# Kernel optimization log

Hardware: AMD Instinct MI355X
Metric: run time of the kernel (lower is better)

## Reference

```python
import jax, jax.numpy as jnp
import numpy as np

B, R, S, H = 4, 64, 512, 768
E = 64            # candidate entities per example
SEG = 128         # seg_emb_dim
NT, NC, NP = 6, 13, 3
REP = 3 * H + 2 * SEG  # rel_rep_size = 2560
NEG = -1e30


def setup_inputs() -> dict:
    key = jax.random.key(0)
    ks = jax.random.split(key, 12)
    hidden_states = jax.random.normal(ks[0], (B, S, H), dtype=jnp.float32)
    rel_pairs = jax.random.randint(ks[1], (B, R, 2), 0, E, dtype=jnp.int64)
    rel_masks = jax.random.randint(ks[2], (B, R, S), 0, 2, dtype=jnp.int32)
    rel_sizes = jax.random.randint(ks[3], (B, R, 2), 0, 30, dtype=jnp.int64)
    ent_span_reps = jax.random.normal(ks[4], (B, E, H), dtype=jnp.float32)
    ent_segs_embs = jax.random.normal(ks[5], (B, E, SEG), dtype=jnp.float32)
    s = 1.0 / np.sqrt(REP)
    W_type = jax.random.uniform(ks[6], (REP, NT), jnp.float32, -s, s)
    b_type = jax.random.uniform(ks[7], (NT,), jnp.float32, -s, s)
    W_cate = jax.random.uniform(ks[8], (REP, NC), jnp.float32, -s, s)
    b_cate = jax.random.uniform(ks[9], (NC,), jnp.float32, -s, s)
    W_pola = jax.random.uniform(ks[10], (REP, NP), jnp.float32, -s, s)
    b_pola = jax.random.uniform(ks[11], (NP,), jnp.float32, -s, s)
    return {"hidden_states": hidden_states, "rel_pairs": rel_pairs,
            "rel_masks": rel_masks, "rel_sizes": rel_sizes,
            "ent_span_reps": ent_span_reps, "ent_segs_embs": ent_segs_embs,
            "W_type": W_type, "b_type": b_type, "W_cate": W_cate,
            "b_cate": b_cate, "W_pola": W_pola, "b_pola": b_pola}


def reference(hidden_states, rel_pairs, rel_masks, rel_sizes,
              ent_span_reps, ent_segs_embs,
              W_type, b_type, W_cate, b_cate, W_pola, b_pola):
    batch, max_rels, _ = rel_pairs.shape
    # batched gather: ent_span_reps[b, rel_pairs[b]] -> [B, R, 2, H] -> [B, R, 2H]
    pair_span = jnp.take_along_axis(
        ent_span_reps[:, :, None, :],
        rel_pairs[:, None, :, :, None].reshape(batch, max_rels * 2, 1, 1), axis=1
    ).reshape(batch, max_rels, -1)
    pair_segs = jnp.take_along_axis(
        ent_segs_embs[:, :, None, :],
        rel_pairs[:, None, :, :, None].reshape(batch, max_rels * 2, 1, 1), axis=1
    ).reshape(batch, max_rels, -1)
    # masked max over seq: scores [B, R, S, H]
    mask_add = (rel_masks == 0).astype(jnp.float32) * NEG          # [B, R, S]
    ctx = jnp.max(hidden_states[:, None, :, :] + mask_add[..., None], axis=2)  # [B, R, H]
    has_ctx = jnp.any(rel_masks != 0, axis=-1)                      # [B, R]
    ctx = jnp.where(has_ctx[..., None], ctx, 0.0)
    features = jnp.concatenate([pair_span, pair_segs, ctx], axis=2)  # [B, R, 2560]
    # dropout is identity at inference
    rel_type_logits = features @ W_type + b_type
    rel_cate_logits = features @ W_cate + b_cate
    rel_pola_logits = features @ W_pola + b_pola
    return (rel_type_logits, rel_cate_logits, rel_pola_logits)
```

## Files before the change

kernel.cpp:

```cpp
#include <hip/hip_runtime.h>
#include <math.h>

#define BB 4
#define RR 64
#define SS 512
#define HH 768
#define EE 64
#define SEGD 128
#define NT 6
#define NC 13
#define NP 3
#define NO (NT + NC + NP)
#define REP 2560
#define RPG 8
#define NGRP (RR / RPG)
#define NEGV -1e30f

template<int ROWS>
__global__ __launch_bounds__(192)
void p1_maxctx(const float* __restrict__ hidden,
               const int*   __restrict__ rel_masks,
               float* __restrict__ ws)
{
    constexpr int SC = SS / ROWS;
    const int bid  = blockIdx.x;
    const int sc   = bid % SC;
    const int grp  = (bid / SC) % NGRP;
    const int b    = bid / (SC * NGRP);
    const int t    = threadIdx.x;
    const int s0   = sc * ROWS;
    const int r0   = grp * RPG;

    __shared__ float sadd[RPG * ROWS];

    for (int i = t; i < RPG * ROWS; i += 192) {
        const int r = i / ROWS;
        const int s = i - r * ROWS;
        const int mv = rel_masks[((size_t)(b * RR + r0 + r)) * SS + s0 + s];
        sadd[i] = mv ? 0.f : NEGV;
    }
    __syncthreads();

    float4 m[RPG];
#pragma unroll
    for (int r = 0; r < RPG; ++r)
        m[r] = make_float4(-INFINITY, -INFINITY, -INFINITY, -INFINITY);

#pragma unroll 8
    for (int s = 0; s < ROWS; ++s) {
        const float4 v = *reinterpret_cast<const float4*>(
            hidden + ((size_t)(b * SS + s0 + s)) * HH + 4 * t);
#pragma unroll
        for (int r = 0; r < RPG; ++r) {
            const float a = sadd[r * ROWS + s];
            m[r].x = fmaxf(m[r].x, v.x + a);
            m[r].y = fmaxf(m[r].y, v.y + a);
            m[r].z = fmaxf(m[r].z, v.z + a);
            m[r].w = fmaxf(m[r].w, v.w + a);
        }
    }

#pragma unroll
    for (int r = 0; r < RPG; ++r) {
        float* wp = ws + (((size_t)(b * RR + r0 + r) * SC) + sc) * HH;
        *reinterpret_cast<float4*>(wp + 4 * t) = m[r];
    }
}

__global__ __launch_bounds__(256)
void p2_head(const float* __restrict__ ws,
             const int*   __restrict__ rel_pairs,
             const float* __restrict__ span,
             const float* __restrict__ segs,
             const float* __restrict__ Wt, const float* __restrict__ bt,
             const float* __restrict__ Wc, const float* __restrict__ bc,
             const float* __restrict__ Wp, const float* __restrict__ bp,
             float* __restrict__ out, int SC)
{
    const int br = blockIdx.x;
    const int b  = br / RR;
    const int t  = threadIdx.x;

    __shared__ float feat[REP];
    __shared__ float red[4][NO];

    const int i0 = rel_pairs[(size_t)br * 2 + 0];
    const int i1 = rel_pairs[(size_t)br * 2 + 1];

    if (t < 192) {
        const float* sp0 = span + ((size_t)b * EE + i0) * HH;
        const float* sp1 = span + ((size_t)b * EE + i1) * HH;
        *reinterpret_cast<float4*>(&feat[4 * t]) =
            *reinterpret_cast<const float4*>(sp0 + 4 * t);
        *reinterpret_cast<float4*>(&feat[HH + 4 * t]) =
            *reinterpret_cast<const float4*>(sp1 + 4 * t);
    } else {
        const int u = t - 192;
        const float* sg = (u < 32) ? (segs + ((size_t)b * EE + i0) * SEGD)
                                   : (segs + ((size_t)b * EE + i1) * SEGD);
        const int v = (u < 32) ? u : (u - 32);
        *reinterpret_cast<float4*>(&feat[2 * HH + ((u < 32) ? 0 : SEGD) + 4 * v]) =
            *reinterpret_cast<const float4*>(sg + 4 * v);
    }

    if (t < 192) {
        float4 mm = make_float4(-INFINITY, -INFINITY, -INFINITY, -INFINITY);
#pragma unroll 4
        for (int c = 0; c < SC; ++c) {
            const float4 w = *reinterpret_cast<const float4*>(
                ws + ((size_t)br * SC + c) * HH + 4 * t);
            mm.x = fmaxf(mm.x, w.x);
            mm.y = fmaxf(mm.y, w.y);
            mm.z = fmaxf(mm.z, w.z);
            mm.w = fmaxf(mm.w, w.w);
        }
        if (mm.x < -1e29f) mm.x = 0.f;
        if (mm.y < -1e29f) mm.y = 0.f;
        if (mm.z < -1e29f) mm.z = 0.f;
        if (mm.w < -1e29f) mm.w = 0.f;
        const int CTX0 = 2 * HH + 2 * SEGD;
        *reinterpret_cast<float4*>(&feat[CTX0 + 4 * t]) = mm;
    }
    __syncthreads();

    float acc[NO];
#pragma unroll
    for (int o = 0; o < NO; ++o) acc[o] = 0.f;
    for (int f = t; f < REP; f += 256) {
        const float fv = feat[f];
        const float* wt = Wt + (size_t)f * NT;
        const float* wc = Wc + (size_t)f * NC;
        const float* wp = Wp + (size_t)f * NP;
#pragma unroll
        for (int o = 0; o < NT; ++o) acc[o]           += fv * wt[o];
#pragma unroll
        for (int o = 0; o < NC; ++o) acc[NT + o]      += fv * wc[o];
#pragma unroll
        for (int o = 0; o < NP; ++o) acc[NT + NC + o] += fv * wp[o];
    }
#pragma unroll
    for (int o = 0; o < NO; ++o) {
#pragma unroll
        for (int off = 32; off > 0; off >>= 1)
            acc[o] += __shfl_down(acc[o], off, 64);
    }
    const int wid  = t >> 6;
    const int lane = t & 63;
    if (lane == 0) {
#pragma unroll
        for (int o = 0; o < NO; ++o) red[wid][o] = acc[o];
    }
    __syncthreads();

    if (t < NO) {
        const float v = red[0][t] + red[1][t] + red[2][t] + red[3][t];
        if (t < NT) {
            out[(size_t)br * NT + t] = v + bt[t];
        } else if (t < NT + NC) {
            const int o = t - NT;
            out[(size_t)BB * RR * NT + (size_t)br * NC + o] = v + bc[o];
        } else {
            const int o = t - NT - NC;
            out[(size_t)BB * RR * (NT + NC) + (size_t)br * NP + o] = v + bp[o];
        }
    }
}

__global__ __launch_bounds__(256)
void rel_cls_fused(const float* __restrict__ hidden,
                   const int*   __restrict__ rel_pairs,
                   const int*   __restrict__ rel_masks,
                   const float* __restrict__ span,
                   const float* __restrict__ segs,
                   const float* __restrict__ Wt, const float* __restrict__ bt,
                   const float* __restrict__ Wc, const float* __restrict__ bc,
                   const float* __restrict__ Wp, const float* __restrict__ bp,
                   float* __restrict__ out)
{
    const int br = blockIdx.x;
    const int b  = br / RR;
    const int t  = threadIdx.x;

    __shared__ float sadd[SS];
    __shared__ float feat[REP];
    __shared__ float red[4][NO];

    const int* mrow = rel_masks + (size_t)br * SS;
    sadd[t]       = mrow[t] ? 0.f : NEGV;
    sadd[t + 256] = mrow[t + 256] ? 0.f : NEGV;

    const int i0 = rel_pairs[(size_t)br * 2 + 0];
    const int i1 = rel_pairs[(size_t)br * 2 + 1];
    const float* sp0 = span + ((size_t)b * EE + i0) * HH;
    const float* sp1 = span + ((size_t)b * EE + i1) * HH;
    feat[t]            = sp0[t];
    feat[t + 256]      = sp0[t + 256];
    feat[t + 512]      = sp0[t + 512];
    feat[HH + t]       = sp1[t];
    feat[HH + t + 256] = sp1[t + 256];
    feat[HH + t + 512] = sp1[t + 512];
    const float* sg0 = segs + ((size_t)b * EE + i0) * SEGD;
    const float* sg1 = segs + ((size_t)b * EE + i1) * SEGD;
    if (t < SEGD) feat[2 * HH + t] = sg0[t];
    else          feat[2 * HH + SEGD + (t - SEGD)] = sg1[t - SEGD];
    __syncthreads();

    float m0 = -INFINITY, m1 = -INFINITY, m2 = -INFINITY;
#pragma unroll 4
    for (int s = 0; s < SS; ++s) {
        const float* hp = hidden + ((size_t)b * SS + s) * HH;
        const float a = sadd[s];
        m0 = fmaxf(m0, hp[t] + a);
        m1 = fmaxf(m1, hp[t + 256] + a);
        m2 = fmaxf(m2, hp[t + 512] + a);
    }
    if (m0 < -1e29f) m0 = 0.f;
    if (m1 < -1e29f) m1 = 0.f;
    if (m2 < -1e29f) m2 = 0.f;
    const int CTX0 = 2 * HH + 2 * SEGD;
    feat[CTX0 + t]       = m0;
    feat[CTX0 + t + 256] = m1;
    feat[CTX0 + t + 512] = m2;
    __syncthreads();

    float acc[NO];
#pragma unroll
    for (int o = 0; o < NO; ++o) acc[o] = 0.f;
    for (int f = t; f < REP; f += 256) {
        const float fv = feat[f];
        const float* wt = Wt + (size_t)f * NT;
        const float* wc = Wc + (size_t)f * NC;
        const float* wp = Wp + (size_t)f * NP;
#pragma unroll
        for (int o = 0; o < NT; ++o) acc[o]           += fv * wt[o];
#pragma unroll
        for (int o = 0; o < NC; ++o) acc[NT + o]      += fv * wc[o];
#pragma unroll
        for (int o = 0; o < NP; ++o) acc[NT + NC + o] += fv * wp[o];
    }
#pragma unroll
    for (int o = 0; o < NO; ++o) {
#pragma unroll
        for (int off = 32; off > 0; off >>= 1)
            acc[o] += __shfl_down(acc[o], off, 64);
    }
    const int wid  = t >> 6;
    const int lane = t & 63;
    if (lane == 0) {
#pragma unroll
        for (int o = 0; o < NO; ++o) red[wid][o] = acc[o];
    }
    __syncthreads();

    if (t < NO) {
        const float v = red[0][t] + red[1][t] + red[2][t] + red[3][t];
        if (t < NT) {
            out[(size_t)br * NT + t] = v + bt[t];
        } else if (t < NT + NC) {
            const int o = t - NT;
            out[(size_t)BB * RR * NT + (size_t)br * NC + o] = v + bc[o];
        } else {
            const int o = t - NT - NC;
            out[(size_t)BB * RR * (NT + NC) + (size_t)br * NP + o] = v + bp[o];
        }
    }
}

extern "C" void kernel_launch(void* const* d_in, const int* in_sizes, int n_in,
                              void* d_out, int out_size, void* d_ws, size_t ws_size,
                              hipStream_t stream) {
    const float* hidden = (const float*)d_in[0];
    const int*   pairs  = (const int*)d_in[1];
    const int*   masks  = (const int*)d_in[2];
    const float* span   = (const float*)d_in[4];
    const float* segs   = (const float*)d_in[5];
    const float* Wt     = (const float*)d_in[6];
    const float* bt     = (const float*)d_in[7];
    const float* Wc     = (const float*)d_in[8];
    const float* bc     = (const float*)d_in[9];
    const float* Wp     = (const float*)d_in[10];
    const float* bp     = (const float*)d_in[11];
    float* out = (float*)d_out;

    const size_t slot = (size_t)BB * RR * HH * sizeof(float);
    float* ws = (float*)d_ws;

    int SC = 0;
    if      ((size_t)32 * slot <= ws_size) SC = 32;
    else if ((size_t)16 * slot <= ws_size) SC = 16;
    else if ((size_t) 8 * slot <= ws_size) SC = 8;
    else if ((size_t) 4 * slot <= ws_size) SC = 4;

    if (SC) {
        dim3 g1(BB * NGRP * SC), b1(192);
        switch (SC) {
            case 32: hipLaunchKernelGGL((p1_maxctx<SS/32>), g1, b1, 0, stream, hidden, masks, ws); break;
            case 16: hipLaunchKernelGGL((p1_maxctx<SS/16>), g1, b1, 0, stream, hidden, masks, ws); break;
            case  8: hipLaunchKernelGGL((p1_maxctx<SS/ 8>), g1, b1, 0, stream, hidden, masks, ws); break;
            default: hipLaunchKernelGGL((p1_maxctx<SS/ 4>), g1, b1, 0, stream, hidden, masks, ws); break;
        }
        dim3 g2(BB * RR), b2(256);
        hipLaunchKernelGGL(p2_head, g2, b2, 0, stream, ws, pairs, span, segs,
                           Wt, bt, Wc, bc, Wp, bp, out, SC);
    } else {
        dim3 grid(BB * RR), blk(256);
        hipLaunchKernelGGL(rel_cls_fused, grid, blk, 0, stream,
                           hidden, pairs, masks, span, segs,
                           Wt, bt, Wc, bc, Wp, bp, out);
    }
}
```

Measured before the change: 33.51 us.

## Transpose classifier weights in phase one and fix split count at sixteen

Extra blocks in the first kernel transpose the three classifier weight matrices into an output-major workspace, so the head kernel can read contiguous float4 weight rows per output instead of strided scalar loads. The masked-max kernel now uses 256 threads with three scalar columns each, and the sequence split is fixed at 16 chunks. Span and segment gathers in the head are moved onto the otherwise idle fourth wave so they overlap the partial-max reduction. The weights are re-transposed on every call, which adds work and workspace traffic to the first kernel, and the two-kernel path now requires a larger workspace.

```diff
diff --git a/kernel.cpp b/kernel.cpp
--- a/kernel.cpp
+++ b/kernel.cpp
@@ -15,55 +15,79 @@
 #define RPG 8
 #define NGRP (RR / RPG)
 #define NEGV -1e30f
-
-template<int ROWS>
-__global__ __launch_bounds__(192)
+#define SCQ 16
+#define ROWS (SS / SCQ)
+#define NB1 (BB * NGRP * SCQ)
+#define NTB 64
+#define WT_ELEMS (REP * NO)
+#define OFF_WT ((size_t)BB * RR * SCQ * HH)
+
+__global__ __launch_bounds__(256)
 void p1_maxctx(const float* __restrict__ hidden,
                const int*   __restrict__ rel_masks,
+               const float* __restrict__ Wt,
+               const float* __restrict__ Wc,
+               const float* __restrict__ Wp,
                float* __restrict__ ws)
 {
-    constexpr int SC = SS / ROWS;
-    const int bid  = blockIdx.x;
-    const int sc   = bid % SC;
-    const int grp  = (bid / SC) % NGRP;
-    const int b    = bid / (SC * NGRP);
-    const int t    = threadIdx.x;
-    const int s0   = sc * ROWS;
-    const int r0   = grp * RPG;
+    const int bid = blockIdx.x;
+    const int t   = threadIdx.x;
+
+    if (bid >= NB1) {
+        float* WT = ws + OFF_WT;
+        for (int e = (bid - NB1) * 256 + t; e < WT_ELEMS; e += NTB * 256) {
+            const int o = e / REP;
+            const int f = e - o * REP;
+            float v;
+            if (o < NT)           v = Wt[(size_t)f * NT + o];
+            else if (o < NT + NC) v = Wc[(size_t)f * NC + (o - NT)];
+            else                  v = Wp[(size_t)f * NP + (o - NT - NC)];
+            WT[e] = v;
+        }
+        return;
+    }
+
+    const int sc  = bid % SCQ;
+    const int grp = (bid / SCQ) % NGRP;
+    const int b   = bid / (SCQ * NGRP);
+    const int s0  = sc * ROWS;
+    const int r0  = grp * RPG;
 
     __shared__ float sadd[RPG * ROWS];
-
-    for (int i = t; i < RPG * ROWS; i += 192) {
-        const int r = i / ROWS;
-        const int s = i - r * ROWS;
+    {
+        const int r = t / ROWS;
+        const int s = t - r * ROWS;
         const int mv = rel_masks[((size_t)(b * RR + r0 + r)) * SS + s0 + s];
-        sadd[i] = mv ? 0.f : NEGV;
-    }
-    __syncthreads();
-
-    float4 m[RPG];
-#pragma unroll
-    for (int r = 0; r < RPG; ++r)
-        m[r] = make_float4(-INFINITY, -INFINITY, -INFINITY, -INFINITY);
-
+        sadd[t] = mv ? 0.f : NEGV;
+    }
+    __syncthreads();
+
+    float m[RPG][3];
+#pragma unroll
+    for (int r = 0; r < RPG; ++r) { m[r][0] = -INFINITY; m[r][1] = -INFINITY; m[r][2] = -INFINITY; }
+
+    const float* hbase = hidden + ((size_t)b * SS + s0) * HH + t;
 #pragma unroll 8
     for (int s = 0; s < ROWS; ++s) {
-        const float4 v = *reinterpret_cast<const float4*>(
-            hidden + ((size_t)(b * SS + s0 + s)) * HH + 4 * t);
+        const float* hp = hbase + (size_t)s * HH;
+        const float v0 = hp[0];
+        const float v1 = hp[256];
+        const float v2 = hp[512];
 #pragma unroll
         for (int r = 0; r < RPG; ++r) {
             const float a = sadd[r * ROWS + s];
-            m[r].x = fmaxf(m[r].x, v.x + a);
-            m[r].y = fmaxf(m[r].y, v.y + a);
-            m[r].z = fmaxf(m[r].z, v.z + a);
-            m[r].w = fmaxf(m[r].w, v.w + a);
+            m[r][0] = fmaxf(m[r][0], v0 + a);
+            m[r][1] = fmaxf(m[r][1], v1 + a);
+            m[r][2] = fmaxf(m[r][2], v2 + a);
         }
     }
 
 #pragma unroll
     for (int r = 0; r < RPG; ++r) {
-        float* wp = ws + (((size_t)(b * RR + r0 + r) * SC) + sc) * HH;
-        *reinterpret_cast<float4*>(wp + 4 * t) = m[r];
+        float* wp = ws + (((size_t)(b * RR + r0 + r)) * SCQ + sc) * HH + t;
+        wp[0]   = m[r][0];
+        wp[256] = m[r][1];
+        wp[512] = m[r][2];
     }
 }
 
@@ -72,10 +96,10 @@
              const int*   __restrict__ rel_pairs,
              const float* __restrict__ span,
              const float* __restrict__ segs,
-             const float* __restrict__ Wt, const float* __restrict__ bt,
-             const float* __restrict__ Wc, const float* __restrict__ bc,
-             const float* __restrict__ Wp, const float* __restrict__ bp,
-             float* __restrict__ out, int SC)
+             const float* __restrict__ bt,
+             const float* __restrict__ bc,
+             const float* __restrict__ bp,
+             float* __restrict__ out)
 {
     const int br = blockIdx.x;
     const int b  = br / RR;
@@ -86,29 +110,14 @@
 
     const int i0 = rel_pairs[(size_t)br * 2 + 0];
     const int i1 = rel_pairs[(size_t)br * 2 + 1];
-
-    if (t < 192) {
-        const float* sp0 = span + ((size_t)b * EE + i0) * HH;
-        const float* sp1 = span + ((size_t)b * EE + i1) * HH;
-        *reinterpret_cast<float4*>(&feat[4 * t]) =
-            *reinterpret_cast<const float4*>(sp0 + 4 * t);
-        *reinterpret_cast<float4*>(&feat[HH + 4 * t]) =
-            *reinterpret_cast<const float4*>(sp1 + 4 * t);
-    } else {
-        const int u = t - 192;
-        const float* sg = (u < 32) ? (segs + ((size_t)b * EE + i0) * SEGD)
-                                   : (segs + ((size_t)b * EE + i1) * SEGD);
-        const int v = (u < 32) ? u : (u - 32);
-        *reinterpret_cast<float4*>(&feat[2 * HH + ((u < 32) ? 0 : SEGD) + 4 * v]) =
-            *reinterpret_cast<const float4*>(sg + 4 * v);
-    }
+    const int CTX0 = 2 * HH + 2 * SEGD;
 
     if (t < 192) {
         float4 mm = make_float4(-INFINITY, -INFINITY, -INFINITY, -INFINITY);
-#pragma unroll 4
-        for (int c = 0; c < SC; ++c) {
-            const float4 w = *reinterpret_cast<const float4*>(
-                ws + ((size_t)br * SC + c) * HH + 4 * t);
+        const float* wbase = ws + (size_t)br * SCQ * HH + 4 * t;
+#pragma unroll
+        for (int c = 0; c < SCQ; ++c) {
+            const float4 w = *reinterpret_cast<const float4*>(wbase + (size_t)c * HH);
             mm.x = fmaxf(mm.x, w.x);
             mm.y = fmaxf(mm.y, w.y);
             mm.z = fmaxf(mm.z, w.z);
@@ -118,26 +127,53 @@
         if (mm.y < -1e29f) mm.y = 0.f;
         if (mm.z < -1e29f) mm.z = 0.f;
         if (mm.w < -1e29f) mm.w = 0.f;
-        const int CTX0 = 2 * HH + 2 * SEGD;
         *reinterpret_cast<float4*>(&feat[CTX0 + 4 * t]) = mm;
-    }
-    __syncthreads();
+    } else {
+        for (int k = t - 192; k < 448; k += 64) {
+            float4 v; int dst;
+            if (k < 192) {
+                v = *reinterpret_cast<const float4*>(span + ((size_t)b * EE + i0) * HH + 4 * k);
+                dst = 4 * k;
+            } else if (k < 384) {
+                const int u = k - 192;
+                v = *reinterpret_cast<const float4*>(span + ((size_t)b * EE + i1) * HH + 4 * u);
+                dst = HH + 4 * u;
+            } else if (k < 416) {
+                const int u = k - 384;
+                v = *reinterpret_cast<const float4*>(segs + ((size_t)b * EE + i0) * SEGD + 4 * u);
+                dst = 2 * HH + 4 * u;
+            } else {
+                const int u = k - 416;
+                v = *reinterpret_cast<const float4*>(segs + ((size_t)b * EE + i1) * SEGD + 4 * u);
+                dst = 2 * HH + SEGD + 4 * u;
+            }
+            *reinterpret_cast<float4*>(&feat[dst]) = v;
+        }
+    }
+    __syncthreads();
+
+    const float* WT = ws + OFF_WT;
+    const float4 f0 = *reinterpret_cast<const float4*>(&feat[4 * t]);
+    const float4 f1 = *reinterpret_cast<const float4*>(&feat[4 * t + 1024]);
+    const bool has2 = (t < 128);
+    float4 f2 = make_float4(0.f, 0.f, 0.f, 0.f);
+    if (has2) f2 = *reinterpret_cast<const float4*>(&feat[4 * t + 2048]);
 
     float acc[NO];
-#pragma unroll
-    for (int o = 0; o < NO; ++o) acc[o] = 0.f;
-    for (int f = t; f < REP; f += 256) {
-        const float fv = feat[f];
-        const float* wt = Wt + (size_t)f * NT;
-        const float* wc = Wc + (size_t)f * NC;
-        const float* wp = Wp + (size_t)f * NP;
-#pragma unroll
-        for (int o = 0; o < NT; ++o) acc[o]           += fv * wt[o];
-#pragma unroll
-        for (int o = 0; o < NC; ++o) acc[NT + o]      += fv * wc[o];
-#pragma unroll
-        for (int o = 0; o < NP; ++o) acc[NT + NC + o] += fv * wp[o];
-    }
+#pragma unroll 4
+    for (int o = 0; o < NO; ++o) {
+        const float* row = WT + (size_t)o * REP + 4 * t;
+        const float4 w0 = *reinterpret_cast<const float4*>(row);
+        const float4 w1 = *reinterpret_cast<const float4*>(row + 1024);
+        float s = f0.x * w0.x + f0.y * w0.y + f0.z * w0.z + f0.w * w0.w
+                + f1.x * w1.x + f1.y * w1.y + f1.z * w1.z + f1.w * w1.w;
+        if (has2) {
+            const float4 w2 = *reinterpret_cast<const float4*>(row + 2048);
+            s += f2.x * w2.x + f2.y * w2.y + f2.z * w2.z + f2.w * w2.w;
+        }
+        acc[o] = s;
+    }
+
 #pragma unroll
     for (int o = 0; o < NO; ++o) {
 #pragma unroll
@@ -206,7 +242,7 @@
     __syncthreads();
 
     float m0 = -INFINITY, m1 = -INFINITY, m2 = -INFINITY;
-#pragma unroll 4
+#pragma unroll 8
     for (int s = 0; s < SS; ++s) {
         const float* hp = hidden + ((size_t)b * SS + s) * HH;
         const float a = sadd[s];
@@ -281,27 +317,17 @@
     const float* Wp     = (const float*)d_in[10];
     const float* bp     = (const float*)d_in[11];
     float* out = (float*)d_out;
-
-    const size_t slot = (size_t)BB * RR * HH * sizeof(float);
-    float* ws = (float*)d_ws;
-
-    int SC = 0;
-    if      ((size_t)32 * slot <= ws_size) SC = 32;
-    else if ((size_t)16 * slot <= ws_size) SC = 16;
-    else if ((size_t) 8 * slot <= ws_size) SC = 8;
-    else if ((size_t) 4 * slot <= ws_size) SC = 4;
-
-    if (SC) {
-        dim3 g1(BB * NGRP * SC), b1(192);
-        switch (SC) {
-            case 32: hipLaunchKernelGGL((p1_maxctx<SS/32>), g1, b1, 0, stream, hidden, masks, ws); break;
-            case 16: hipLaunchKernelGGL((p1_maxctx<SS/16>), g1, b1, 0, stream, hidden, masks, ws); break;
-            case  8: hipLaunchKernelGGL((p1_maxctx<SS/ 8>), g1, b1, 0, stream, hidden, masks, ws); break;
-            default: hipLaunchKernelGGL((p1_maxctx<SS/ 4>), g1, b1, 0, stream, hidden, masks, ws); break;
-        }
-        dim3 g2(BB * RR), b2(256);
-        hipLaunchKernelGGL(p2_head, g2, b2, 0, stream, ws, pairs, span, segs,
-                           Wt, bt, Wc, bc, Wp, bp, out, SC);
+    float* ws  = (float*)d_ws;
+
+    const size_t need = (OFF_WT + (size_t)WT_ELEMS) * sizeof(float);
+
+    if (ws_size >= need) {
+        dim3 g1(NB1 + NTB), blk(256);
+        hipLaunchKernelGGL(p1_maxctx, g1, blk, 0, stream,
+                           hidden, masks, Wt, Wc, Wp, ws);
+        dim3 g2(BB * RR);
+        hipLaunchKernelGGL(p2_head, g2, blk, 0, stream,
+                           ws, pairs, span, segs, bt, bc, bp, out);
     } else {
         dim3 grid(BB * RR), blk(256);
         hipLaunchKernelGGL(rel_cls_fused, grid, blk, 0, stream,
```

Result: slower. 35.34 us (+5.5%).
